# Kernel tuning notes

Measured on AMD Instinct MI355X. Metric: run time of the kernel, lower is better.

## Reference

```python
import jax, jax.numpy as jnp
import numpy as np

B, T, N, H = 32, 512, 32, 128  # batch, time, num_series (== num_chans), hidden


def setup_inputs() -> dict:
    key = jax.random.key(0)
    ks = jax.random.split(key, 7)
    s = 1.0 / np.sqrt(H)  # PyTorch LSTM default init range
    X = jax.random.normal(ks[0], (B, T, N), dtype=jnp.float32)
    W_ih = jax.random.uniform(ks[1], (N, 4 * H, N), minval=-s, maxval=s, dtype=jnp.float32)
    W_hh = jax.random.uniform(ks[2], (N, 4 * H, H), minval=-s, maxval=s, dtype=jnp.float32)
    b_ih = jax.random.uniform(ks[3], (N, 4 * H), minval=-s, maxval=s, dtype=jnp.float32)
    b_hh = jax.random.uniform(ks[4], (N, 4 * H), minval=-s, maxval=s, dtype=jnp.float32)
    W_out = jax.random.uniform(ks[5], (N, H), minval=-s, maxval=s, dtype=jnp.float32)  # Conv1d(hidden,1,1) weight per series
    b_out = jax.random.uniform(ks[6], (N,), minval=-s, maxval=s, dtype=jnp.float32)
    return dict(X=X, W_ih=W_ih, W_hh=W_hh, b_ih=b_ih, b_hh=b_hh, W_out=W_out, b_out=b_out)


def reference(X, W_ih, W_hh, b_ih, b_hh, W_out, b_out):
    """Ensemble of N independent single-layer LSTMs over the same input X,
    each followed by a 1x1 conv (linear) head; outputs concatenated on dim 2.
    Gate order follows PyTorch: i, f, g, o."""
    Bsz, Tlen, P = X.shape
    Nser, _, Hid = W_hh.shape
    # Precompute input projections for all series/timesteps: [T, N, B, 4H]
    xproj = jnp.einsum('btp,ngp->tnbg', X, W_ih) + (b_ih + b_hh)[None, :, None, :]
    h0 = jnp.zeros((Nser, Bsz, Hid), X.dtype)
    c0 = jnp.zeros((Nser, Bsz, Hid), X.dtype)

    def step(carry, xt):
        h, c = carry
        gates = xt + jnp.einsum('nbh,ngh->nbg', h, W_hh)  # [N,B,4H]
        i, f, g, o = jnp.split(gates, 4, axis=-1)
        c = jax.nn.sigmoid(f) * c + jax.nn.sigmoid(i) * jnp.tanh(g)
        h = jax.nn.sigmoid(o) * jnp.tanh(c)
        return (h, c), h

    (hT, cT), hs = jax.lax.scan(step, (h0, c0), xproj)  # hs: [T, N, B, H]
    # 1x1 conv head per series, then concatenate along series dim -> [B, T, N]
    pred = jnp.einsum('tnbh,nh->btn', hs, W_out) + b_out[None, None, :]
    return pred, hT, cT
```

## Files before the change

### kernel.cpp

```cpp
#include <hip/hip_runtime.h>
#include <hip/hip_bf16.h>

typedef __attribute__((ext_vector_type(8))) short s16x8;
typedef __attribute__((ext_vector_type(4))) float f32x4;

#define MFMA_B16(a, b, c) __builtin_amdgcn_mfma_f32_16x16x32_bf16((a), (b), (c), 0, 0, 0)

static __device__ __forceinline__ short f2bf(float f) {
    __hip_bfloat16 h = __float2bfloat16(f);
    return __builtin_bit_cast(short, h);
}
static __device__ __forceinline__ float rcp_f(float x) {
    return __builtin_amdgcn_rcpf(x);
}

__global__ void xcvt_kernel(const float* __restrict__ X, short* __restrict__ Xb, int n) {
    int i = (blockIdx.x * 256 + threadIdx.x) * 4;
    if (i < n) {
        float4 v = *(const float4*)(X + i);
        short4 o;
        o.x = f2bf(v.x); o.y = f2bf(v.y); o.z = f2bf(v.z); o.w = f2bf(v.w);
        *(short4*)(Xb + i) = o;
    }
}

template<bool BF16X>
__global__ __launch_bounds__(512, 2)
void clstm_kernel(const float* __restrict__ X,
                  const short* __restrict__ Xb,
                  const float* __restrict__ W_ih,
                  const float* __restrict__ W_hh,
                  const float* __restrict__ b_ih,
                  const float* __restrict__ b_hh,
                  const float* __restrict__ W_out,
                  const float* __restrict__ b_out,
                  float* __restrict__ out)
{
    constexpr int B = 32, T = 512, N = 32, H = 128, G = 512;
    constexpr int HT_OFF = B * T * N;
    constexpr int CT_OFF = HT_OFF + N * B * H;
    constexpr int PRED_OFF = 8192;
    constexpr float C1 = 1.4426950408889634f;

    __shared__ __align__(16) unsigned char smem[16384];

    const int tid  = threadIdx.x;
    const int w    = tid >> 6;
    const int L    = tid & 63;
    const int col  = L & 15;
    const int quad = L >> 4;
    const int n    = blockIdx.x & 31;
    const int bgrp = blockIdx.x >> 5;

    s16x8 Bh[4][4];
    s16x8 Bx[4];
    f32x4 biasv[4];
#pragma unroll
    for (int tt = 0; tt < 4; ++tt) {
        const int g = (w + 8 * tt) * 16 + col;
        const float* whr = W_hh + ((size_t)n * G + g) * H + quad * 8;
#pragma unroll
        for (int kt = 0; kt < 4; ++kt) {
            const float* p = whr + kt * 32;
#pragma unroll
            for (int jj = 0; jj < 8; ++jj) Bh[tt][kt][jj] = f2bf(p[jj]);
        }
        const float* wir = W_ih + ((size_t)n * G + g) * N + quad * 8;
#pragma unroll
        for (int jj = 0; jj < 8; ++jj) Bx[tt][jj] = f2bf(wir[jj]);
        const float bb = b_ih[n * G + g] + b_hh[n * G + g];
        biasv[tt] = (f32x4){bb, bb, bb, bb};
    }

    s16x8 Bp[4];
    const float bo = b_out[n];
    const f32x4 bov = (f32x4){bo, bo, bo, bo};
#pragma unroll
    for (int kt = 0; kt < 4; ++kt) {
        const float* wp = W_out + n * H + kt * 32 + quad * 8;
#pragma unroll
        for (int jj = 0; jj < 8; ++jj)
            Bp[kt][jj] = (col == 0) ? f2bf(wp[jj]) : (short)0;
    }

    int wboff;
    {
        const int j = w * 16 + col;
        wboff = (j >> 5) * 1024 + (((((j >> 3) & 3) << 4) | (quad << 2)) * 16) + (j & 7) * 2;
    }

    const bool xactive = (col & 3) == 0;
    const int  xb      = bgrp * 4 + (col >> 2);
    const float* xp  = X + ((size_t)xb * T) * N + quad * 8;
    const short* xbp = BF16X ? (Xb + ((size_t)xb * T) * N + quad * 8) : nullptr;

    auto loadx = [&](int t) -> s16x8 {
        s16x8 r = (s16x8)(short)0;
        if (xactive) {
            if constexpr (BF16X) {
                r = *(const s16x8*)(xbp + (size_t)t * N);
            } else {
                float4 lo = *(const float4*)(xp + (size_t)t * N);
                float4 hi = *(const float4*)(xp + (size_t)t * N + 4);
                r[0] = f2bf(lo.x); r[1] = f2bf(lo.y); r[2] = f2bf(lo.z); r[3] = f2bf(lo.w);
                r[4] = f2bf(hi.x); r[5] = f2bf(hi.y); r[6] = f2bf(hi.z); r[7] = f2bf(hi.w);
            }
        }
        return r;
    };

    *(float4*)(smem + tid * 16)        = make_float4(0.f, 0.f, 0.f, 0.f);
    *(float4*)(smem + 8192 + tid * 16) = make_float4(0.f, 0.f, 0.f, 0.f);

    float cst = 0.f, hlast = 0.f;

    f32x4 accA[4], accB[4];
    {
        s16x8 x0 = loadx(0);
#pragma unroll
        for (int tt = 0; tt < 4; ++tt)
            accA[tt] = MFMA_B16(x0, Bx[tt], biasv[tt]);
    }
    s16x8 xA = loadx(1);
    s16x8 xB = loadx(2);

    __syncthreads();

#define STEP(P, TCUR, CUR, NXT)                                                     \
    {                                                                               \
        const unsigned char* rb = smem + (P) * 4096;                                \
        s16x8 Af[4];                                                                \
        _Pragma("unroll")                                                           \
        for (int kt = 0; kt < 4; ++kt)                                              \
            Af[kt] = *(const s16x8*)(rb + kt * 1024 + L * 16);                      \
                 \
        _Pragma("unroll")                                                           \
        for (int tt = 0; tt < 4; ++tt)                                              \
            NXT[tt] = MFMA_B16(xA, Bx[tt], biasv[tt]);                              \
                 \
        xA = xB;                                                                    \
        xB = loadx(((TCUR) + 3 < T) ? (TCUR) + 3 : T - 1);                          \
                \
        _Pragma("unroll")                                                           \
        for (int tt = 0; tt < 4; ++tt)                                              \
            CUR[tt] = MFMA_B16(Af[0], Bh[tt][0], CUR[tt]);                          \
        _Pragma("unroll")                                                           \
        for (int kt = 1; kt < 4; ++kt) {                                            \
            _Pragma("unroll")                                                       \
            for (int tt = 0; tt < 4; ++tt)                                          \
                CUR[tt] = MFMA_B16(Af[kt], Bh[tt][kt], CUR[tt]);                    \
        }                                                                           \
        if (w == ((TCUR) & 7)) {                                                    \
            f32x4 pacc = bov;                                                       \
            _Pragma("unroll")                                                       \
            for (int kt = 0; kt < 4; ++kt)                                          \
                pacc = MFMA_B16(Af[kt], Bp[kt], pacc);                              \
            if ((TCUR) > 0 && col == 0)                                             \
                *(float*)(smem + PRED_OFF + ((quad << 9) + (TCUR) - 1) * 4) =       \
                    pacc[0];                                                        \
        }                                                                           \
                                     \
        {                                                                           \
            const float iv = CUR[0][0], fv = CUR[1][0];                             \
            const float gv = CUR[2][0], ov = CUR[3][0];                             \
            const float ei = exp2f(-C1 * iv);                                       \
            const float ef = exp2f(-C1 * fv);                                       \
            const float eg = exp2f(-2.0f * C1 * gv);                                \
            const float eo = exp2f(-C1 * ov);                                       \
            const float sf = rcp_f(1.0f + ef);                                      \
            const float itg = (1.0f - eg) * rcp_f((1.0f + ei) * (1.0f + eg));       \
            const float cc = __builtin_fmaf(sf, cst, itg);                          \
            cst = cc;                                                               \
            const float ec = exp2f(-2.0f * C1 * cc);                                \
            const float hv = (1.0f - ec) * rcp_f((1.0f + eo) * (1.0f + ec));        \
            hlast = hv;                                                             \
            *(short*)(smem + ((P) ^ 1) * 4096 + wboff) = f2bf(hv);                  \
        }                                                                           \
        __syncthreads();                                                            \
    }

#pragma unroll 1
    for (int t2 = 0; t2 < T; t2 += 2) {
        STEP(0, t2, accA, accB)
        STEP(1, t2 + 1, accB, accA)
    }
#undef STEP

    if (w == 0) {
        f32x4 pacc = bov;
#pragma unroll
        for (int kt = 0; kt < 4; ++kt) {
            s16x8 Af = *(const s16x8*)(smem + kt * 1024 + L * 16);
            pacc = MFMA_B16(Af, Bp[kt], pacc);
        }
        if (col == 0)
            *(float*)(smem + PRED_OFF + ((quad << 9) + (T - 1)) * 4) = pacc[0];
    }
    __syncthreads();

#pragma unroll
    for (int e = tid; e < 4 * T; e += 512) {
        const int b = e >> 9, t = e & (T - 1);
        out[((size_t)(bgrp * 4 + b) * T + t) * N + n] =
            *(const float*)(smem + PRED_OFF + e * 4);
    }

    {
        const int bglob = bgrp * 4 + quad;
        const int j = w * 16 + col;
        out[HT_OFF + ((size_t)n * B + bglob) * H + j] = hlast;
        out[CT_OFF + ((size_t)n * B + bglob) * H + j] = cst;
    }
}

extern "C" void kernel_launch(void* const* d_in, const int* in_sizes, int n_in,
                              void* d_out, int out_size, void* d_ws, size_t ws_size,
                              hipStream_t stream) {
    const float* X     = (const float*)d_in[0];
    const float* W_ih  = (const float*)d_in[1];
    const float* W_hh  = (const float*)d_in[2];
    const float* b_ih  = (const float*)d_in[3];
    const float* b_hh  = (const float*)d_in[4];
    const float* W_out = (const float*)d_in[5];
    const float* b_out = (const float*)d_in[6];
    float* out = (float*)d_out;

    const int xelems = 32 * 512 * 32;
    const bool usebf = ws_size >= (size_t)xelems * sizeof(short);

    if (usebf) {
        short* Xb = (short*)d_ws;
        xcvt_kernel<<<dim3(xelems / 1024), dim3(256), 0, stream>>>(X, Xb, xelems);
        clstm_kernel<true><<<dim3(256), dim3(512), 0, stream>>>(
            X, Xb, W_ih, W_hh, b_ih, b_hh, W_out, b_out, out);
    } else {
        clstm_kernel<false><<<dim3(256), dim3(512), 0, stream>>>(
            X, nullptr, W_ih, W_hh, b_ih, b_hh, W_out, b_out, out);
    }
}
```

Baseline: 362.4 us.

## Compact hidden-state LDS buffer and split MFMA accumulation chains

The hidden-state exchange buffer shrinks from 4KB to 1KB per phase. Only the rows that hold real batch entries (col%4==0) are stored and read, and the other A-fragment lanes are zero-filled in registers instead of loaded from padded shared memory. The recurrent K-reduction is split into two independent MFMA accumulator chains that are summed before the gate nonlinearities, which shortens the dependent MFMA latency chain. This lowers LDS traffic and footprint per step at the cost of a few extra adds and some branching on lane activity.

```diff
diff --git a/kernel.cpp b/kernel.cpp
--- a/kernel.cpp
+++ b/kernel.cpp
@@ -39,10 +39,10 @@
     constexpr int B = 32, T = 512, N = 32, H = 128, G = 512;
     constexpr int HT_OFF = B * T * N;
     constexpr int CT_OFF = HT_OFF + N * B * H;
-    constexpr int PRED_OFF = 8192;
+    constexpr int PRED_OFF = 2048;
     constexpr float C1 = 1.4426950408889634f;
 
-    __shared__ __align__(16) unsigned char smem[16384];
+    __shared__ __align__(16) unsigned char smem[2048 + 8192];
 
     const int tid  = threadIdx.x;
     const int w    = tid >> 6;
@@ -75,6 +75,7 @@
     s16x8 Bp[4];
     const float bo = b_out[n];
     const f32x4 bov = (f32x4){bo, bo, bo, bo};
+    const f32x4 z4  = (f32x4){0.f, 0.f, 0.f, 0.f};
 #pragma unroll
     for (int kt = 0; kt < 4; ++kt) {
         const float* wp = W_out + n * H + kt * 32 + quad * 8;
@@ -86,7 +87,7 @@
     int wboff;
     {
         const int j = w * 16 + col;
-        wboff = (j >> 5) * 1024 + (((((j >> 3) & 3) << 4) | (quad << 2)) * 16) + (j & 7) * 2;
+        wboff = ((j >> 5) << 8) + (((j >> 3) & 3) << 6) + (quad << 4) + ((j & 7) << 1);
     }
 
     const bool xactive = (col & 3) == 0;
@@ -109,8 +110,7 @@
         return r;
     };
 
-    *(float4*)(smem + tid * 16)        = make_float4(0.f, 0.f, 0.f, 0.f);
-    *(float4*)(smem + 8192 + tid * 16) = make_float4(0.f, 0.f, 0.f, 0.f);
+    if (tid < 64) *(float4*)(smem + tid * 16) = make_float4(0.f, 0.f, 0.f, 0.f);
 
     float cst = 0.f, hlast = 0.f;
 
@@ -128,27 +128,30 @@
 
 #define STEP(P, TCUR, CUR, NXT)                                                     \
     {                                                                               \
-        const unsigned char* rb = smem + (P) * 4096;                                \
+        const unsigned char* rb = smem + (P) * 1024;                                \
         s16x8 Af[4];                                                                \
         _Pragma("unroll")                                                           \
-        for (int kt = 0; kt < 4; ++kt)                                              \
-            Af[kt] = *(const s16x8*)(rb + kt * 1024 + L * 16);                      \
-                 \
+        for (int kt = 0; kt < 4; ++kt) Af[kt] = (s16x8)(short)0;                    \
+        if (xactive) {                                                              \
+            const unsigned char* ra = rb + (quad << 6) + ((col >> 2) << 4);         \
+            _Pragma("unroll")                                                       \
+            for (int kt = 0; kt < 4; ++kt)                                          \
+                Af[kt] = *(const s16x8*)(ra + kt * 256);                            \
+        }                                                                           \
+                      \
         _Pragma("unroll")                                                           \
         for (int tt = 0; tt < 4; ++tt)                                              \
             NXT[tt] = MFMA_B16(xA, Bx[tt], biasv[tt]);                              \
-                 \
         xA = xB;                                                                    \
         xB = loadx(((TCUR) + 3 < T) ? (TCUR) + 3 : T - 1);                          \
-                \
+                             \
+        f32x4 acc2[4];                                                              \
         _Pragma("unroll")                                                           \
-        for (int tt = 0; tt < 4; ++tt)                                              \
-            CUR[tt] = MFMA_B16(Af[0], Bh[tt][0], CUR[tt]);                          \
-        _Pragma("unroll")                                                           \
-        for (int kt = 1; kt < 4; ++kt) {                                            \
-            _Pragma("unroll")                                                       \
-            for (int tt = 0; tt < 4; ++tt)                                          \
-                CUR[tt] = MFMA_B16(Af[kt], Bh[tt][kt], CUR[tt]);                    \
+        for (int tt = 0; tt < 4; ++tt) {                                            \
+            CUR[tt]  = MFMA_B16(Af[0], Bh[tt][0], CUR[tt]);                         \
+            acc2[tt] = MFMA_B16(Af[2], Bh[tt][2], z4);                              \
+            CUR[tt]  = MFMA_B16(Af[1], Bh[tt][1], CUR[tt]);                         \
+            acc2[tt] = MFMA_B16(Af[3], Bh[tt][3], acc2[tt]);                        \
         }                                                                           \
         if (w == ((TCUR) & 7)) {                                                    \
             f32x4 pacc = bov;                                                       \
@@ -161,8 +164,10 @@
         }                                                                           \
                                      \
         {                                                                           \
-            const float iv = CUR[0][0], fv = CUR[1][0];                             \
-            const float gv = CUR[2][0], ov = CUR[3][0];                             \
+            const float iv = CUR[0][0] + acc2[0][0];                                \
+            const float fv = CUR[1][0] + acc2[1][0];                                \
+            const float gv = CUR[2][0] + acc2[2][0];                                \
+            const float ov = CUR[3][0] + acc2[3][0];                                \
             const float ei = exp2f(-C1 * iv);                                       \
             const float ef = exp2f(-C1 * fv);                                       \
             const float eg = exp2f(-2.0f * C1 * gv);                                \
@@ -174,7 +179,7 @@
             const float ec = exp2f(-2.0f * C1 * cc);                                \
             const float hv = (1.0f - ec) * rcp_f((1.0f + eo) * (1.0f + ec));        \
             hlast = hv;                                                             \
-            *(short*)(smem + ((P) ^ 1) * 4096 + wboff) = f2bf(hv);                  \
+            *(short*)(smem + ((P) ^ 1) * 1024 + wboff) = f2bf(hv);                  \
         }                                                                           \
         __syncthreads();                                                            \
     }
@@ -188,11 +193,18 @@
 
     if (w == 0) {
         f32x4 pacc = bov;
-#pragma unroll
-        for (int kt = 0; kt < 4; ++kt) {
-            s16x8 Af = *(const s16x8*)(smem + kt * 1024 + L * 16);
-            pacc = MFMA_B16(Af, Bp[kt], pacc);
+        s16x8 Af[4];
+#pragma unroll
+        for (int kt = 0; kt < 4; ++kt) Af[kt] = (s16x8)(short)0;
+        if (xactive) {
+            const unsigned char* ra = smem + (quad << 6) + ((col >> 2) << 4);
+#pragma unroll
+            for (int kt = 0; kt < 4; ++kt)
+                Af[kt] = *(const s16x8*)(ra + kt * 256);
         }
+#pragma unroll
+        for (int kt = 0; kt < 4; ++kt)
+            pacc = MFMA_B16(Af[kt], Bp[kt], pacc);
         if (col == 0)
             *(float*)(smem + PRED_OFF + ((quad << 9) + (T - 1)) * 4) = pacc[0];
     }
```

Result: slower. 470.3 us (+29.8%).

## Fuse X bf16 conversion into LSTM kernel and stage all timesteps in LDS

Applied to the files above, without the earlier changes.

Adds a fused kernel that loads the block's full X slice (4 batches × 512 timesteps) from global memory, converts it to bf16 and stores it in 128KB of dynamic shared memory before the recurrence. Per-step input loads then come from LDS instead of global memory, and the separate conversion kernel launch goes away. The cost is a large LDS footprint (~144KB per block), which may limit residency to one block per CU, plus an upfront load phase before the serial recurrence begins. It falls back to the old path if the shared-memory attribute cannot be set.

```diff
diff --git a/kernel.cpp b/kernel.cpp
--- a/kernel.cpp
+++ b/kernel.cpp
@@ -21,6 +21,194 @@
         short4 o;
         o.x = f2bf(v.x); o.y = f2bf(v.y); o.z = f2bf(v.z); o.w = f2bf(v.w);
         *(short4*)(Xb + i) = o;
+    }
+}
+
+__global__ __launch_bounds__(512, 2)
+void clstm_fused(const float* __restrict__ X,
+                 const float* __restrict__ W_ih,
+                 const float* __restrict__ W_hh,
+                 const float* __restrict__ b_ih,
+                 const float* __restrict__ b_hh,
+                 const float* __restrict__ W_out,
+                 const float* __restrict__ b_out,
+                 float* __restrict__ out)
+{
+    constexpr int B = 32, T = 512, N = 32, H = 128, G = 512;
+    constexpr int HT_OFF = B * T * N;
+    constexpr int CT_OFF = HT_OFF + N * B * H;
+    constexpr int PRED_OFF = 8192;
+    constexpr int XOFF = 16384;
+    constexpr float C1 = 1.4426950408889634f;
+
+    extern __shared__ __align__(16) unsigned char smem[];
+
+    const int tid  = threadIdx.x;
+    const int w    = tid >> 6;
+    const int L    = tid & 63;
+    const int col  = L & 15;
+    const int quad = L >> 4;
+    const int n    = blockIdx.x & 31;
+    const int bgrp = blockIdx.x >> 5;
+
+    s16x8 Bh[4][4];
+    s16x8 Bx[4];
+    f32x4 biasv[4];
+#pragma unroll
+    for (int tt = 0; tt < 4; ++tt) {
+        const int g = (w + 8 * tt) * 16 + col;
+        const float* whr = W_hh + ((size_t)n * G + g) * H + quad * 8;
+#pragma unroll
+        for (int kt = 0; kt < 4; ++kt) {
+            const float* p = whr + kt * 32;
+#pragma unroll
+            for (int jj = 0; jj < 8; ++jj) Bh[tt][kt][jj] = f2bf(p[jj]);
+        }
+        const float* wir = W_ih + ((size_t)n * G + g) * N + quad * 8;
+#pragma unroll
+        for (int jj = 0; jj < 8; ++jj) Bx[tt][jj] = f2bf(wir[jj]);
+        const float bb = b_ih[n * G + g] + b_hh[n * G + g];
+        biasv[tt] = (f32x4){bb, bb, bb, bb};
+    }
+
+    s16x8 Bp[4];
+    const float bo = b_out[n];
+    const f32x4 bov = (f32x4){bo, bo, bo, bo};
+#pragma unroll
+    for (int kt = 0; kt < 4; ++kt) {
+        const float* wp = W_out + n * H + kt * 32 + quad * 8;
+#pragma unroll
+        for (int jj = 0; jj < 8; ++jj)
+            Bp[kt][jj] = (col == 0) ? f2bf(wp[jj]) : (short)0;
+    }
+
+    int wboff;
+    {
+        const int j = w * 16 + col;
+        wboff = (j >> 5) * 1024 + (((((j >> 3) & 3) << 4) | (quad << 2)) * 16) + (j & 7) * 2;
+    }
+
+    const bool xactive = (col & 3) == 0;
+    const int  xlbase  = XOFF + ((col >> 2) << 6) + (quad << 4);
+
+    auto loadx = [&](int t) -> s16x8 {
+        s16x8 r = (s16x8)(short)0;
+        if (xactive)
+            r = *(const s16x8*)(smem + xlbase + t * 256);
+        return r;
+    };
+
+    *(float4*)(smem + tid * 16)        = make_float4(0.f, 0.f, 0.f, 0.f);
+    *(float4*)(smem + 8192 + tid * 16) = make_float4(0.f, 0.f, 0.f, 0.f);
+    {
+        const int bgrp4 = bgrp * 4;
+#pragma unroll 8
+        for (int k = 0; k < 32; ++k) {
+            const int e4 = (tid + (k << 9)) << 2;
+            const int p4 = e4 & 31;
+            const int t  = (e4 >> 5) & 511;
+            const int bl = e4 >> 14;
+            const float4 v = *(const float4*)(X + ((size_t)(bgrp4 + bl) * T + t) * N + p4);
+            short4 o;
+            o.x = f2bf(v.x); o.y = f2bf(v.y); o.z = f2bf(v.z); o.w = f2bf(v.w);
+            *(short4*)(smem + XOFF + t * 256 + bl * 64 + p4 * 2) = o;
+        }
+    }
+    __syncthreads();
+
+    float cst = 0.f, hlast = 0.f;
+
+    f32x4 accA[4], accB[4];
+    {
+        s16x8 x0 = loadx(0);
+#pragma unroll
+        for (int tt = 0; tt < 4; ++tt)
+            accA[tt] = MFMA_B16(x0, Bx[tt], biasv[tt]);
+    }
+    s16x8 xA = loadx(1);
+    s16x8 xB = loadx(2);
+
+#define STEP(P, TCUR, CUR, NXT)                                                     \
+    {                                                                               \
+        const unsigned char* rb = smem + (P) * 4096;                                \
+        s16x8 Af[4];                                                                \
+        _Pragma("unroll")                                                           \
+        for (int kt = 0; kt < 4; ++kt)                                              \
+            Af[kt] = *(const s16x8*)(rb + kt * 1024 + L * 16);                      \
+        _Pragma("unroll")                                                           \
+        for (int tt = 0; tt < 4; ++tt)                                              \
+            NXT[tt] = MFMA_B16(xA, Bx[tt], biasv[tt]);                              \
+        xA = xB;                                                                    \
+        xB = loadx(((TCUR) + 3 < T) ? (TCUR) + 3 : T - 1);                          \
+        _Pragma("unroll")                                                           \
+        for (int tt = 0; tt < 4; ++tt)                                              \
+            CUR[tt] = MFMA_B16(Af[0], Bh[tt][0], CUR[tt]);                          \
+        _Pragma("unroll")                                                           \
+        for (int kt = 1; kt < 4; ++kt) {                                            \
+            _Pragma("unroll")                                                       \
+            for (int tt = 0; tt < 4; ++tt)                                          \
+                CUR[tt] = MFMA_B16(Af[kt], Bh[tt][kt], CUR[tt]);                    \
+        }                                                                           \
+        if (w == ((TCUR) & 7)) {                                                    \
+            f32x4 pacc = bov;                                                       \
+            _Pragma("unroll")                                                       \
+            for (int kt = 0; kt < 4; ++kt)                                          \
+                pacc = MFMA_B16(Af[kt], Bp[kt], pacc);                              \
+            if ((TCUR) > 0 && col == 0)                                             \
+                *(float*)(smem + PRED_OFF + ((quad << 9) + (TCUR) - 1) * 4) =       \
+                    pacc[0];                                                        \
+        }                                                                           \
+                                     \
+        {                                                                           \
+            const float iv = CUR[0][0], fv = CUR[1][0];                             \
+            const float gv = CUR[2][0], ov = CUR[3][0];                             \
+            const float ei = exp2f(-C1 * iv);                                       \
+            const float ef = exp2f(-C1 * fv);                                       \
+            const float eg = exp2f(-2.0f * C1 * gv);                                \
+            const float eo = exp2f(-C1 * ov);                                       \
+            const float sf = rcp_f(1.0f + ef);                                      \
+            const float itg = (1.0f - eg) * rcp_f((1.0f + ei) * (1.0f + eg));       \
+            const float cc = __builtin_fmaf(sf, cst, itg);                          \
+            cst = cc;                                                               \
+            const float ec = exp2f(-2.0f * C1 * cc);                                \
+            const float hv = (1.0f - ec) * rcp_f((1.0f + eo) * (1.0f + ec));        \
+            hlast = hv;                                                             \
+            *(short*)(smem + ((P) ^ 1) * 4096 + wboff) = f2bf(hv);                  \
+        }                                                                           \
+        __syncthreads();                                                            \
+    }
+
+#pragma unroll 1
+    for (int t2 = 0; t2 < T; t2 += 2) {
+        STEP(0, t2, accA, accB)
+        STEP(1, t2 + 1, accB, accA)
+    }
+#undef STEP
+
+    if (w == 0) {
+        f32x4 pacc = bov;
+#pragma unroll
+        for (int kt = 0; kt < 4; ++kt) {
+            s16x8 Af = *(const s16x8*)(smem + kt * 1024 + L * 16);
+            pacc = MFMA_B16(Af, Bp[kt], pacc);
+        }
+        if (col == 0)
+            *(float*)(smem + PRED_OFF + ((quad << 9) + (T - 1)) * 4) = pacc[0];
+    }
+    __syncthreads();
+
+#pragma unroll
+    for (int e = tid; e < 4 * T; e += 512) {
+        const int b = e >> 9, t = e & (T - 1);
+        out[((size_t)(bgrp * 4 + b) * T + t) * N + n] =
+            *(const float*)(smem + PRED_OFF + e * 4);
+    }
+
+    {
+        const int bglob = bgrp * 4 + quad;
+        const int j = w * 16 + col;
+        out[HT_OFF + ((size_t)n * B + bglob) * H + j] = hlast;
+        out[CT_OFF + ((size_t)n * B + bglob) * H + j] = cst;
     }
 }
 
@@ -133,14 +321,11 @@
         _Pragma("unroll")                                                           \
         for (int kt = 0; kt < 4; ++kt)                                              \
             Af[kt] = *(const s16x8*)(rb + kt * 1024 + L * 16);                      \
-                 \
         _Pragma("unroll")                                                           \
         for (int tt = 0; tt < 4; ++tt)                                              \
             NXT[tt] = MFMA_B16(xA, Bx[tt], biasv[tt]);                              \
-                 \
         xA = xB;                                                                    \
         xB = loadx(((TCUR) + 3 < T) ? (TCUR) + 3 : T - 1);                          \
-                \
         _Pragma("unroll")                                                           \
         for (int tt = 0; tt < 4; ++tt)                                              \
             CUR[tt] = MFMA_B16(Af[0], Bh[tt][0], CUR[tt]);                          \
@@ -159,7 +344,6 @@
                 *(float*)(smem + PRED_OFF + ((quad << 9) + (TCUR) - 1) * 4) =       \
                     pacc[0];                                                        \
         }                                                                           \
-                                     \
         {                                                                           \
             const float iv = CUR[0][0], fv = CUR[1][0];                             \
             const float gv = CUR[2][0], ov = CUR[3][0];                             \
@@ -225,16 +409,30 @@
     const float* b_out = (const float*)d_in[6];
     float* out = (float*)d_out;
 
-    const int xelems = 32 * 512 * 32;
-    const bool usebf = ws_size >= (size_t)xelems * sizeof(short);
-
-    if (usebf) {
-        short* Xb = (short*)d_ws;
-        xcvt_kernel<<<dim3(xelems / 1024), dim3(256), 0, stream>>>(X, Xb, xelems);
-        clstm_kernel<true><<<dim3(256), dim3(512), 0, stream>>>(
-            X, Xb, W_ih, W_hh, b_ih, b_hh, W_out, b_out, out);
+    constexpr int SMEM_BYTES = 16384 + 131072;
+
+    static int mode = -1;
+    if (mode < 0) {
+        hipError_t e = hipFuncSetAttribute(
+            reinterpret_cast<const void*>(&clstm_fused),
+            hipFuncAttributeMaxDynamicSharedMemorySize, SMEM_BYTES);
+        mode = (e == hipSuccess) ? 1 : 0;
+    }
+
+    if (mode) {
+        clstm_fused<<<dim3(256), dim3(512), SMEM_BYTES, stream>>>(
+            X, W_ih, W_hh, b_ih, b_hh, W_out, b_out, out);
     } else {
-        clstm_kernel<false><<<dim3(256), dim3(512), 0, stream>>>(
-            X, nullptr, W_ih, W_hh, b_ih, b_hh, W_out, b_out, out);
-    }
-}
+        const int xelems = 32 * 512 * 32;
+        const bool usebf = ws_size >= (size_t)xelems * sizeof(short);
+        if (usebf) {
+            short* Xb = (short*)d_ws;
+            xcvt_kernel<<<dim3(xelems / 1024), dim3(256), 0, stream>>>(X, Xb, xelems);
+            clstm_kernel<true><<<dim3(256), dim3(512), 0, stream>>>(
+                X, Xb, W_ih, W_hh, b_ih, b_hh, W_out, b_out, out);
+        } else {
+            clstm_kernel<false><<<dim3(256), dim3(512), 0, stream>>>(
+                X, nullptr, W_ih, W_hh, b_ih, b_hh, W_out, b_out, out);
+        }
+    }
+}
```

After: 364.1 us. No clear change (+0.5%).
